# Kernel optimization log

Hardware: AMD Instinct MI355X
Metric: run time of the kernel (lower is better)

The kernel has to match this reference:

```python
import jax, jax.numpy as jnp
import numpy as np

STRIDE, PADDING, EPS = 2, 1, 1e-5


def setup_inputs() -> dict:
    key = jax.random.key(0)
    k1, k2, k3 = jax.random.split(key, 3)
    C_in, C_out, K = 64, 64, 4
    x = jax.random.normal(k1, (32, C_in, 64, 64), dtype=jnp.float32)
    weight = jax.random.normal(k2, (C_in, C_out, K, K), dtype=jnp.float32) * 0.05  # torch layout (in,out,kh,kw)
    conv_bias = jax.random.normal(k3, (C_out,), dtype=jnp.float32) * 0.02
    gamma = jnp.ones((C_out,), dtype=jnp.float32)
    beta = jnp.zeros((C_out,), dtype=jnp.float32)
    running_mean = jnp.zeros((C_out,), dtype=jnp.float32)
    running_var = jnp.ones((C_out,), dtype=jnp.float32)
    return {"x": x, "weight": weight, "conv_bias": conv_bias, "gamma": gamma,
            "beta": beta, "running_mean": running_mean, "running_var": running_var}


def _conv_transpose2d(x, weight, bias, stride, padding):
    # torch.nn.functional.conv_transpose2d equivalent:
    # conv with lhs_dilation=stride, spatially-flipped kernel, in/out axes swapped,
    # and padding k-1-p on each side.
    k = weight.shape[2]
    w_t = jnp.transpose(jnp.flip(weight, (2, 3)), (1, 0, 2, 3))  # (Cout, Cin, k, k)
    pad = k - 1 - padding
    y = jax.lax.conv_general_dilated(
        x, w_t,
        window_strides=(1, 1),
        padding=[(pad, pad), (pad, pad)],
        lhs_dilation=(stride, stride),
        dimension_numbers=("NCHW", "OIHW", "NCHW"),
    )
    return y + bias[None, :, None, None]


def reference(x, weight, conv_bias, gamma, beta, running_mean, running_var):
    # ConvTranspose2d
    y = _conv_transpose2d(x, weight, conv_bias, STRIDE, PADDING)  # [N,C,128,128]
    # BatchNorm2d (inference, running stats)
    scale = gamma * jax.lax.rsqrt(running_var + EPS)
    y = (y - running_mean[None, :, None, None]) * scale[None, :, None, None] + beta[None, :, None, None]
    # Softmax over channel dim
    y = jax.nn.softmax(y, axis=1)
    # MaxPool2d(k=2, s=2): H,W are even, so reshape-max is exact
    N, C, H, W = y.shape
    y = y.reshape(N, C, H // 2, 2, W // 2, 2).max(axis=(3, 5))  # [N,C,64,64]
    return y
```

## Files before the change

### kernel.cpp

```cpp
#include <hip/hip_runtime.h>
#include <hip/hip_bf16.h>
#include <math.h>


typedef __attribute__((ext_vector_type(8))) short short8;
typedef __attribute__((ext_vector_type(4))) float floatx4;

#define COLS 66

__device__ ushort g_wfrag[4 * 8 * 4 * 64 * 8];
__device__ float g_aff[64];

__device__ __forceinline__ ushort f2bf(float f) {
  union { float f; unsigned u; } v; v.f = f;
  unsigned r = v.u + 0x7FFF + ((v.u >> 16) & 1);
  return (ushort)(r >> 16);
}

__global__ __launch_bounds__(256) void prep_kernel(
    const float* __restrict__ w, const float* __restrict__ bias,
    const float* __restrict__ gamma, const float* __restrict__ beta,
    const float* __restrict__ mean, const float* __restrict__ var) {
  int t = blockIdx.x * 256 + threadIdx.x;
  int cin0 = (t >> 6) * 2;
  int cout = t & 63;
  int nt = cout >> 4, b15 = cout & 15;
  int q = (cin0 & 31) >> 3;
  int j = cin0 & 7;
  int ksq = cin0 >> 5;
  float A = gamma[cout] * rsqrtf(var[cout] + 1e-5f);

  const float4* p0 = (const float4*)&w[(cin0 * 64 + cout) * 16];
  const float4* p1 = (const float4*)&w[((cin0 + 1) * 64 + cout) * 16];
  float a[16], b[16];
  {
    float4 f0 = p0[0], f1 = p0[1], f2 = p0[2], f3 = p0[3];
    a[0]=f0.x; a[1]=f0.y; a[2]=f0.z; a[3]=f0.w; a[4]=f1.x; a[5]=f1.y; a[6]=f1.z; a[7]=f1.w;
    a[8]=f2.x; a[9]=f2.y; a[10]=f2.z; a[11]=f2.w; a[12]=f3.x; a[13]=f3.y; a[14]=f3.z; a[15]=f3.w;
    float4 g0 = p1[0], g1 = p1[1], g2 = p1[2], g3 = p1[3];
    b[0]=g0.x; b[1]=g0.y; b[2]=g0.z; b[3]=g0.w; b[4]=g1.x; b[5]=g1.y; b[6]=g1.z; b[7]=g1.w;
    b[8]=g2.x; b[9]=g2.y; b[10]=g2.z; b[11]=g2.w; b[12]=g3.x; b[13]=g3.y; b[14]=g3.z; b[15]=g3.w;
  }
#pragma unroll
  for (int kh = 0; kh < 4; ++kh)
#pragma unroll
    for (int kw = 0; kw < 4; ++kw) {
      int r = (kh & 1) ? 0 : 1;
      int pp = (kw & 1) ? 0 : 1;
      int c = r * 2 + pp;
      int tap = (kh >> 1) * 2 + (kw >> 1);
      int ks = tap * 2 + ksq;
      unsigned u = (unsigned)f2bf(a[kh * 4 + kw] * A) |
                   ((unsigned)f2bf(b[kh * 4 + kw] * A) << 16);
      *(unsigned*)&g_wfrag[(((c * 8 + ks) * 4 + nt) * 64 + q * 16 + b15) * 8 + j] = u;
    }

  if (t < 64) {
    float Ai = gamma[t] * rsqrtf(var[t] + 1e-5f);
    g_aff[t] = (bias[t] - mean[t]) * Ai + beta[t];
  }
}

__global__ __launch_bounds__(256, 4) void fused_kernel(const float* __restrict__ x,
                                                       float* __restrict__ out) {
  __shared__ ushort xs[4 * COLS * 64];

  const int tid  = threadIdx.x;
  const int ph0  = blockIdx.x * 2;
  const int n    = blockIdx.y;
  const int wave = tid >> 6;
  const int lane = tid & 63;
  const int b15  = lane & 15;
  const int q    = lane >> 4;
  const int wr   = wave >> 1;
  const int wc   = wave & 1;

  for (int e = tid; e < 4 * 16 * 16; e += 256) {
    int iw4 = e & 15;
    int c4  = (e >> 4) & 15;
    int row = e >> 8;
    int ih  = ph0 - 1 + row;
    float4 v0 = {0.f, 0.f, 0.f, 0.f}, v1 = v0, v2 = v0, v3 = v0;
    if (ih >= 0 && ih < 64) {
      const float* xp = x + ((n * 64 + c4 * 4) * 64 + ih) * 64 + iw4 * 4;
      v0 = *(const float4*)xp;          v1 = *(const float4*)(xp + 4096);
      v2 = *(const float4*)(xp + 8192); v3 = *(const float4*)(xp + 12288);
    }
    int chunk = c4 >> 1, half4 = (c4 & 1) * 4;
    float cc[4][4] = {{v0.x, v1.x, v2.x, v3.x}, {v0.y, v1.y, v2.y, v3.y},
                      {v0.z, v1.z, v2.z, v3.z}, {v0.w, v1.w, v2.w, v3.w}};
#pragma unroll
    for (int ii = 0; ii < 4; ++ii) {
      int col = iw4 * 4 + ii + 1;
      __hip_bfloat162 lo = __float22bfloat162_rn({cc[ii][0], cc[ii][1]});
      __hip_bfloat162 hi = __float22bfloat162_rn({cc[ii][2], cc[ii][3]});
      ushort4 pk = {*(ushort*)&lo.x, *(ushort*)&lo.y, *(ushort*)&hi.x, *(ushort*)&hi.y};
      *(ushort4*)&xs[(row * COLS + col) * 64 + ((chunk ^ (col & 7)) * 8) + half4] = pk;
    }
  }
  for (int e = tid; e < 4 * 2 * 16; e += 256) {
    int c4 = e & 15, side = (e >> 4) & 1, row = e >> 5;
    int col = side ? 65 : 0;
    int chunk = c4 >> 1, half4 = (c4 & 1) * 4;
    ushort4 z; z.x = z.y = z.z = z.w = 0;
    *(ushort4*)&xs[(row * COLS + col) * 64 + ((chunk ^ (col & 7)) * 8) + half4] = z;
  }
  __syncthreads();

  float Dc[4];
#pragma unroll
  for (int nt = 0; nt < 4; ++nt) Dc[nt] = g_aff[nt * 16 + b15];

  floatx4 pooled[8];
#pragma unroll
  for (int i = 0; i < 8; ++i) pooled[i] = (floatx4){0.f, 0.f, 0.f, 0.f};

  short8 bfA[4], bfB[4];
  {
    const short8* wf = (const short8*)g_wfrag;
#pragma unroll
    for (int nt = 0; nt < 4; ++nt) bfA[nt] = wf[nt * 64 + lane];
  }

  for (int c = 0; c < 4; ++c) {
    const int r = c >> 1, p = c & 1;
    floatx4 acc[8];
#pragma unroll
    for (int i = 0; i < 8; ++i) acc[i] = (floatx4){0.f, 0.f, 0.f, 0.f};

#pragma unroll
    for (int ks = 0; ks < 8; ++ks) {
      short8* cur = (ks & 1) ? bfB : bfA;
      short8* nxt = (ks & 1) ? bfA : bfB;
      if (ks < 7) {
        const short8* wf = (const short8*)g_wfrag + (c * 8 + ks + 1) * 256;
#pragma unroll
        for (int nt = 0; nt < 4; ++nt) nxt[nt] = wf[nt * 64 + lane];
      } else if (c < 3) {
        const short8* wf = (const short8*)g_wfrag + (c + 1) * 8 * 256;
#pragma unroll
        for (int nt = 0; nt < 4; ++nt) nxt[nt] = wf[nt * 64 + lane];
      }
      const int a = ks >> 2, b = (ks >> 1) & 1;
      const int hrow = wr + (r ? (a ? 1 : 2) : (a ? 0 : 1));
      const int dx   = p ? (b ? 0 : 1) : (b ? -1 : 0);
      const int chunk = (ks & 1) * 4 + q;
      short8 af[2];
#pragma unroll
      for (int mt = 0; mt < 2; ++mt) {
        int col = wc * 32 + mt * 16 + b15 + dx + 1;
        af[mt] = *(const short8*)&xs[(hrow * COLS + col) * 64 + ((chunk ^ (col & 7)) * 8)];
      }
#pragma unroll
      for (int nt = 0; nt < 4; ++nt)
#pragma unroll
        for (int mt = 0; mt < 2; ++mt)
          acc[mt * 4 + nt] =
              __builtin_amdgcn_mfma_f32_16x16x32_bf16(af[mt], cur[nt], acc[mt * 4 + nt], 0, 0, 0);
    }

#pragma unroll
    for (int mt = 0; mt < 2; ++mt) {
      float sm[4] = {0.f, 0.f, 0.f, 0.f};
#pragma unroll
      for (int nt = 0; nt < 4; ++nt)
#pragma unroll
        for (int reg = 0; reg < 4; ++reg) {
          float e = __expf(acc[mt * 4 + nt][reg] + Dc[nt]);
          acc[mt * 4 + nt][reg] = e;
          sm[reg] += e;
        }
#pragma unroll
      for (int reg = 0; reg < 4; ++reg) {
        sm[reg] += __shfl_xor(sm[reg], 1, 64);
        sm[reg] += __shfl_xor(sm[reg], 2, 64);
        sm[reg] += __shfl_xor(sm[reg], 4, 64);
        sm[reg] += __shfl_xor(sm[reg], 8, 64);
        sm[reg] = 1.0f / sm[reg];
      }
#pragma unroll
      for (int nt = 0; nt < 4; ++nt)
#pragma unroll
        for (int reg = 0; reg < 4; ++reg)
          pooled[mt * 4 + nt][reg] =
              fmaxf(pooled[mt * 4 + nt][reg], acc[mt * 4 + nt][reg] * sm[reg]);
    }
  }

  __syncthreads();
  float* red = (float*)xs;
#pragma unroll
  for (int mt = 0; mt < 2; ++mt)
#pragma unroll
    for (int nt = 0; nt < 4; ++nt)
#pragma unroll
      for (int reg = 0; reg < 4; ++reg)
        red[(wr * 64 + nt * 16 + b15) * 66 + wc * 32 + mt * 16 + q * 4 + reg] =
            pooled[mt * 4 + nt][reg];
  __syncthreads();
  for (int e = tid; e < 4096; e += 256) {
    int pw2  = e & 31;
    int cout = (e >> 5) & 63;
    int rl   = e >> 11;
    float2 val = *(float2*)&red[(rl * 64 + cout) * 66 + pw2 * 2];
    *(float2*)&out[((n * 64 + cout) * 64 + (ph0 + rl)) * 64 + pw2 * 2] = val;
  }
}

extern "C" void kernel_launch(void* const* d_in, const int* in_sizes, int n_in,
                              void* d_out, int out_size, void* d_ws, size_t ws_size,
                              hipStream_t stream) {
  const float* x     = (const float*)d_in[0];
  const float* w     = (const float*)d_in[1];
  const float* bias  = (const float*)d_in[2];
  const float* gamma = (const float*)d_in[3];
  const float* beta  = (const float*)d_in[4];
  const float* mean  = (const float*)d_in[5];
  const float* var   = (const float*)d_in[6];
  float* out = (float*)d_out;

  prep_kernel<<<8, 256, 0, stream>>>(w, bias, gamma, beta, mean, var);
  dim3 grid(32, 32);
  fused_kernel<<<grid, 256, 0, stream>>>(x, out);
}
```

Baseline: 120.8 us.

## Enlarge block tile to four pooled rows with fp16 pooled accumulators

```diff
diff --git a/kernel.cpp b/kernel.cpp
--- a/kernel.cpp
+++ b/kernel.cpp
@@ -1,10 +1,10 @@
 #include <hip/hip_runtime.h>
-#include <hip/hip_bf16.h>
 #include <math.h>
 
 
 typedef __attribute__((ext_vector_type(8))) short short8;
 typedef __attribute__((ext_vector_type(4))) float floatx4;
+typedef _Float16 __attribute__((ext_vector_type(2))) h2;
 
 #define COLS 66
 
@@ -15,6 +15,13 @@
   union { float f; unsigned u; } v; v.f = f;
   unsigned r = v.u + 0x7FFF + ((v.u >> 16) & 1);
   return (ushort)(r >> 16);
+}
+
+__device__ __forceinline__ h2 h2max(h2 a, h2 b) {
+  h2 r;
+  r.x = (a.x > b.x) ? a.x : b.x;
+  r.y = (a.y > b.y) ? a.y : b.y;
+  return r;
 }
 
 __global__ __launch_bounds__(256) void prep_kernel(
@@ -61,49 +68,45 @@
   }
 }
 
-__global__ __launch_bounds__(256, 4) void fused_kernel(const float* __restrict__ x,
+__global__ __launch_bounds__(256, 2) void fused_kernel(const float* __restrict__ x,
                                                        float* __restrict__ out) {
-  __shared__ ushort xs[4 * COLS * 64];
+  __shared__ ushort xs[6 * COLS * 64];
 
   const int tid  = threadIdx.x;
-  const int ph0  = blockIdx.x * 2;
+  const int ph0  = blockIdx.x * 4;
   const int n    = blockIdx.y;
   const int wave = tid >> 6;
   const int lane = tid & 63;
   const int b15  = lane & 15;
   const int q    = lane >> 4;
-  const int wr   = wave >> 1;
-  const int wc   = wave & 1;
-
-  for (int e = tid; e < 4 * 16 * 16; e += 256) {
-    int iw4 = e & 15;
-    int c4  = (e >> 4) & 15;
-    int row = e >> 8;
-    int ih  = ph0 - 1 + row;
-    float4 v0 = {0.f, 0.f, 0.f, 0.f}, v1 = v0, v2 = v0, v3 = v0;
-    if (ih >= 0 && ih < 64) {
-      const float* xp = x + ((n * 64 + c4 * 4) * 64 + ih) * 64 + iw4 * 4;
-      v0 = *(const float4*)xp;          v1 = *(const float4*)(xp + 4096);
-      v2 = *(const float4*)(xp + 8192); v3 = *(const float4*)(xp + 12288);
-    }
-    int chunk = c4 >> 1, half4 = (c4 & 1) * 4;
-    float cc[4][4] = {{v0.x, v1.x, v2.x, v3.x}, {v0.y, v1.y, v2.y, v3.y},
-                      {v0.z, v1.z, v2.z, v3.z}, {v0.w, v1.w, v2.w, v3.w}};
-#pragma unroll
-    for (int ii = 0; ii < 4; ++ii) {
-      int col = iw4 * 4 + ii + 1;
-      __hip_bfloat162 lo = __float22bfloat162_rn({cc[ii][0], cc[ii][1]});
-      __hip_bfloat162 hi = __float22bfloat162_rn({cc[ii][2], cc[ii][3]});
-      ushort4 pk = {*(ushort*)&lo.x, *(ushort*)&lo.y, *(ushort*)&hi.x, *(ushort*)&hi.y};
-      *(ushort4*)&xs[(row * COLS + col) * 64 + ((chunk ^ (col & 7)) * 8) + half4] = pk;
-    }
-  }
-  for (int e = tid; e < 4 * 2 * 16; e += 256) {
-    int c4 = e & 15, side = (e >> 4) & 1, row = e >> 5;
-    int col = side ? 65 : 0;
-    int chunk = c4 >> 1, half4 = (c4 & 1) * 4;
-    ushort4 z; z.x = z.y = z.z = z.w = 0;
-    *(ushort4*)&xs[(row * COLS + col) * 64 + ((chunk ^ (col & 7)) * 8) + half4] = z;
+
+  {
+    const int col = lane + 1;
+#pragma unroll
+    for (int i = 0; i < 12; ++i) {
+      int pairidx = i * 4 + wave;
+      int row = pairidx >> 3;
+      int chunk = pairidx & 7;
+      int ih = ph0 - 1 + row;
+      float f[8] = {0.f, 0.f, 0.f, 0.f, 0.f, 0.f, 0.f, 0.f};
+      if (ih >= 0 && ih < 64) {
+        const float* xp = x + ((n * 64 + chunk * 8) * 64 + ih) * 64 + lane;
+#pragma unroll
+        for (int jj = 0; jj < 8; ++jj) f[jj] = xp[jj * 4096];
+      }
+      int4 pk;
+      pk.x = (int)f2bf(f[0]) | ((int)f2bf(f[1]) << 16);
+      pk.y = (int)f2bf(f[2]) | ((int)f2bf(f[3]) << 16);
+      pk.z = (int)f2bf(f[4]) | ((int)f2bf(f[5]) << 16);
+      pk.w = (int)f2bf(f[6]) | ((int)f2bf(f[7]) << 16);
+      *(int4*)&xs[(row * COLS + col) * 64 + ((chunk ^ (col & 7)) * 8)] = pk;
+    }
+  }
+  if (tid < 96) {
+    int chunk = tid & 7, side = (tid >> 3) & 1, row = tid >> 4;
+    int colp = side ? 65 : 0;
+    int4 z = {0, 0, 0, 0};
+    *(int4*)&xs[(row * COLS + colp) * 64 + ((chunk ^ (colp & 7)) * 8)] = z;
   }
   __syncthreads();
 
@@ -111,9 +114,9 @@
 #pragma unroll
   for (int nt = 0; nt < 4; ++nt) Dc[nt] = g_aff[nt * 16 + b15];
 
-  floatx4 pooled[8];
-#pragma unroll
-  for (int i = 0; i < 8; ++i) pooled[i] = (floatx4){0.f, 0.f, 0.f, 0.f};
+  h2 pooled[32];
+#pragma unroll
+  for (int i = 0; i < 32; ++i) pooled[i] = (h2){(_Float16)0.f, (_Float16)0.f};
 
   short8 bfA[4], bfB[4];
   {
@@ -122,11 +125,12 @@
     for (int nt = 0; nt < 4; ++nt) bfA[nt] = wf[nt * 64 + lane];
   }
 
+#pragma unroll
   for (int c = 0; c < 4; ++c) {
     const int r = c >> 1, p = c & 1;
-    floatx4 acc[8];
-#pragma unroll
-    for (int i = 0; i < 8; ++i) acc[i] = (floatx4){0.f, 0.f, 0.f, 0.f};
+    floatx4 acc[16];
+#pragma unroll
+    for (int i = 0; i < 16; ++i) acc[i] = (floatx4){0.f, 0.f, 0.f, 0.f};
 
 #pragma unroll
     for (int ks = 0; ks < 8; ++ks) {
@@ -142,25 +146,25 @@
         for (int nt = 0; nt < 4; ++nt) nxt[nt] = wf[nt * 64 + lane];
       }
       const int a = ks >> 2, b = (ks >> 1) & 1;
-      const int hrow = wr + (r ? (a ? 1 : 2) : (a ? 0 : 1));
+      const int hrow = wave + (r ? (a ? 1 : 2) : (a ? 0 : 1));
       const int dx   = p ? (b ? 0 : 1) : (b ? -1 : 0);
       const int chunk = (ks & 1) * 4 + q;
-      short8 af[2];
-#pragma unroll
-      for (int mt = 0; mt < 2; ++mt) {
-        int col = wc * 32 + mt * 16 + b15 + dx + 1;
+      short8 af[4];
+#pragma unroll
+      for (int mt = 0; mt < 4; ++mt) {
+        int col = mt * 16 + b15 + dx + 1;
         af[mt] = *(const short8*)&xs[(hrow * COLS + col) * 64 + ((chunk ^ (col & 7)) * 8)];
       }
 #pragma unroll
       for (int nt = 0; nt < 4; ++nt)
 #pragma unroll
-        for (int mt = 0; mt < 2; ++mt)
+        for (int mt = 0; mt < 4; ++mt)
           acc[mt * 4 + nt] =
               __builtin_amdgcn_mfma_f32_16x16x32_bf16(af[mt], cur[nt], acc[mt * 4 + nt], 0, 0, 0);
     }
 
 #pragma unroll
-    for (int mt = 0; mt < 2; ++mt) {
+    for (int mt = 0; mt < 4; ++mt) {
       float sm[4] = {0.f, 0.f, 0.f, 0.f};
 #pragma unroll
       for (int nt = 0; nt < 4; ++nt)
@@ -179,31 +183,43 @@
         sm[reg] = 1.0f / sm[reg];
       }
 #pragma unroll
-      for (int nt = 0; nt < 4; ++nt)
-#pragma unroll
-        for (int reg = 0; reg < 4; ++reg)
-          pooled[mt * 4 + nt][reg] =
-              fmaxf(pooled[mt * 4 + nt][reg], acc[mt * 4 + nt][reg] * sm[reg]);
+      for (int nt = 0; nt < 4; ++nt) {
+        h2 p01 = {(_Float16)(acc[mt * 4 + nt][0] * sm[0]),
+                  (_Float16)(acc[mt * 4 + nt][1] * sm[1])};
+        h2 p23 = {(_Float16)(acc[mt * 4 + nt][2] * sm[2]),
+                  (_Float16)(acc[mt * 4 + nt][3] * sm[3])};
+        pooled[(mt * 4 + nt) * 2 + 0] = h2max(pooled[(mt * 4 + nt) * 2 + 0], p01);
+        pooled[(mt * 4 + nt) * 2 + 1] = h2max(pooled[(mt * 4 + nt) * 2 + 1], p23);
+      }
     }
   }
 
   __syncthreads();
   float* red = (float*)xs;
 #pragma unroll
-  for (int mt = 0; mt < 2; ++mt)
-#pragma unroll
-    for (int nt = 0; nt < 4; ++nt)
-#pragma unroll
-      for (int reg = 0; reg < 4; ++reg)
-        red[(wr * 64 + nt * 16 + b15) * 66 + wc * 32 + mt * 16 + q * 4 + reg] =
-            pooled[mt * 4 + nt][reg];
-  __syncthreads();
-  for (int e = tid; e < 4096; e += 256) {
-    int pw2  = e & 31;
-    int cout = (e >> 5) & 63;
-    int rl   = e >> 11;
-    float2 val = *(float2*)&red[(rl * 64 + cout) * 66 + pw2 * 2];
-    *(float2*)&out[((n * 64 + cout) * 64 + (ph0 + rl)) * 64 + pw2 * 2] = val;
+  for (int half = 0; half < 2; ++half) {
+    if ((wave >> 1) == half) {
+      int rl = wave & 1;
+#pragma unroll
+      for (int mt = 0; mt < 4; ++mt)
+#pragma unroll
+        for (int nt = 0; nt < 4; ++nt) {
+          h2 lo = pooled[(mt * 4 + nt) * 2 + 0];
+          h2 hi = pooled[(mt * 4 + nt) * 2 + 1];
+          float* rp = &red[(rl * 64 + nt * 16 + b15) * 66 + mt * 16 + q * 4];
+          rp[0] = (float)lo.x; rp[1] = (float)lo.y;
+          rp[2] = (float)hi.x; rp[3] = (float)hi.y;
+        }
+    }
+    __syncthreads();
+    for (int e = tid; e < 4096; e += 256) {
+      int pw2  = e & 31;
+      int cout = (e >> 5) & 63;
+      int rl   = e >> 11;
+      float2 val = *(float2*)&red[(rl * 64 + cout) * 66 + pw2 * 2];
+      *(float2*)&out[((n * 64 + cout) * 64 + (ph0 + half * 2 + rl)) * 64 + pw2 * 2] = val;
+    }
+    __syncthreads();
   }
 }
 
@@ -220,6 +236,6 @@
   float* out = (float*)d_out;
 
   prep_kernel<<<8, 256, 0, stream>>>(w, bias, gamma, beta, mean, var);
-  dim3 grid(32, 32);
+  dim3 grid(16, 32);
   fused_kernel<<<grid, 256, 0, stream>>>(x, out);
 }
```

After: 165.2 us. 1.37x slower.
